# Performance work log

Hardware: AMD Instinct MI355X
Metric: run time of the kernel (lower is better)

## Reference

```python
import jax, jax.numpy as jnp
import numpy as np

ETA = 0.01   # nudging rate from __init__ default
EPS = 1e-8   # cosine-similarity epsilon


def setup_inputs() -> dict:
    key = jax.random.key(0)
    ks = jax.random.split(key, 6)
    B, F, S, E, D = 64, 512, 8192, 500000, 1024
    return {
        "heatmap_features_batch": jax.random.normal(ks[0], (B, F), dtype=jnp.float32),
        "grad_output_batch": jax.random.normal(ks[1], (B, F), dtype=jnp.float32),
        "sign_features": jax.random.normal(ks[2], (S, F), dtype=jnp.float32),
        "edge_weight": jax.random.uniform(ks[3], (E,), dtype=jnp.float32),
        "edge_disease": jax.random.randint(ks[4], (E,), 0, D, dtype=jnp.int32),
        "edge_sign": jax.random.randint(ks[5], (E,), 0, S, dtype=jnp.int32),
        "num_diseases": D,
    }


def reference(heatmap_features_batch, grad_output_batch, sign_features,
              edge_weight, edge_disease, edge_sign, num_diseases):
    # Cosine similarity between every sample's heatmap feature vector and every
    # sign node's stored feature vector, rescaled to [0, 1].
    Hn = heatmap_features_batch / (
        jnp.linalg.norm(heatmap_features_batch, axis=1, keepdims=True) + EPS)
    Sn = sign_features / (
        jnp.linalg.norm(sign_features, axis=1, keepdims=True) + EPS)
    sim = (jnp.einsum('bf,sf->bs', Hn, Sn) + 1.0) * 0.5          # [B, S]

    # Per-edge weighted similarity, gathered at each edge's sign node.
    contrib = sim[:, edge_sign] * edge_weight[None, :]           # [B, E]

    # Scatter-add edge contributions into the disease (source) index.
    agg = jax.ops.segment_sum(contrib.T, edge_disease,
                              num_segments=num_diseases)         # [D, B]

    # Per-sample gradient norm factor g^(i) = ||grad_i||_2.
    gnorm = jnp.linalg.norm(grad_output_batch, axis=1)           # [B]

    return ETA * gnorm[:, None] * agg.T                          # [B, D]
```

## Files before the change

kernel.cpp:

```cpp
#include <hip/hip_runtime.h>
#include <math.h>

#define EPS 1e-8f
#define SCB 256
#define NG1 128
#define CAP 768

typedef __attribute__((ext_vector_type(8))) __bf16 bf16x8;
typedef __attribute__((ext_vector_type(4))) float f32x4;

__device__ __forceinline__ unsigned short f2bf(float x) {
    unsigned int u = __float_as_uint(x);
    u += 0x7FFFu + ((u >> 16) & 1u);
    return (unsigned short)(u >> 16);
}
__device__ __forceinline__ unsigned int pack2(float lo, float hi) {
    return (unsigned int)f2bf(lo) | ((unsigned int)f2bf(hi) << 16);
}

__global__ __launch_bounds__(256) void k_norms(
        const float* __restrict__ Sg, const float* __restrict__ Hg,
        const float* __restrict__ Gg, unsigned short* __restrict__ Sgb,
        unsigned short* __restrict__ Hsb, float* __restrict__ gscale,
        int* __restrict__ cursor, int Srows, int Fdim, int Bdim, int Dd) {
    __shared__ float redA[4][17];
    __shared__ float redB[4][17];
    int bid = blockIdx.x;
    int tid = threadIdx.x;
    int lane = tid & 63, wv = tid >> 6;
    int r = tid & 15, cg = tid >> 4;
    int nsT = Srows >> 4;

    if (bid < nsT + (Bdim >> 4)) {
        bool isH = bid >= nsT;
        int t = isH ? bid - nsT : bid;
        const float* basep = isH ? Hg : Sg;
        const float4* src = (const float4*)(basep + ((size_t)t * 16 + r) * Fdim);

        float4 v[8];
        float ss = 0.f, sgq = 0.f;
        #pragma unroll
        for (int g = 0; g < 4; g++) {
            int c = cg + g * 16;
            float4 x = src[c * 2], y = src[c * 2 + 1];
            v[2 * g] = x; v[2 * g + 1] = y;
            ss += x.x * x.x + x.y * x.y + x.z * x.z + x.w * x.w
                + y.x * y.x + y.y * y.y + y.z * y.z + y.w * y.w;
        }
        if (isH) {
            const float4* srcg = (const float4*)(Gg + ((size_t)t * 16 + r) * Fdim);
            #pragma unroll
            for (int g = 0; g < 4; g++) {
                int c = cg + g * 16;
                float4 x = srcg[c * 2], y = srcg[c * 2 + 1];
                sgq += x.x * x.x + x.y * x.y + x.z * x.z + x.w * x.w
                     + y.x * y.x + y.y * y.y + y.z * y.z + y.w * y.w;
            }
        }
        ss  += __shfl_xor(ss, 16, 64);  ss  += __shfl_xor(ss, 32, 64);
        sgq += __shfl_xor(sgq, 16, 64); sgq += __shfl_xor(sgq, 32, 64);
        if (lane < 16) { redA[wv][lane] = ss; redB[wv][lane] = sgq; }
        __syncthreads();
        float tot = redA[0][r] + redA[1][r] + redA[2][r] + redA[3][r];
        float rv = 1.0f / (sqrtf(tot) + EPS);
        if (isH && tid < 16) {
            float tg = redB[0][tid] + redB[1][tid] + redB[2][tid] + redB[3][tid];
            gscale[t * 16 + tid] = 0.005f * sqrtf(tg);
        }
        uint4* dp = (uint4*)(isH ? Hsb : Sgb);
        #pragma unroll
        for (int g = 0; g < 4; g++) {
            int c = cg + g * 16;
            uint4 o;
            o.x = pack2(v[2 * g].x * rv,     v[2 * g].y * rv);
            o.y = pack2(v[2 * g].z * rv,     v[2 * g].w * rv);
            o.z = pack2(v[2 * g + 1].x * rv, v[2 * g + 1].y * rv);
            o.w = pack2(v[2 * g + 1].z * rv, v[2 * g + 1].w * rv);
            dp[(size_t)t * 1024 + (size_t)c * 16 + r] = o;
        }
    } else {
        for (int i = tid; i < Dd; i += 256) cursor[i] = 0;
    }
}

__global__ __launch_bounds__(256) void k_g1scat(
        const unsigned short* __restrict__ Sgb,
        const unsigned short* __restrict__ Hsb, float* __restrict__ Pt,
        const int* __restrict__ ed, const int* __restrict__ es,
        const float* __restrict__ ew, int* __restrict__ cursor,
        int2* __restrict__ sorted, int Srows, int Fdim, int E, int Dd) {
    __shared__ int cnt[1024];
    int id = blockIdx.x;
    int tid = threadIdx.x;

    if (id < NG1) {
        int lane = tid & 63, w = tid >> 6;
        int wt = id * 4 + w;
        const bf16x8* A  = (const bf16x8*)Sgb + (size_t)wt * 1024 + lane;
        const bf16x8* Bp = (const bf16x8*)Hsb + lane;

        f32x4 acc0 = {0.f, 0.f, 0.f, 0.f};
        f32x4 acc1 = {0.f, 0.f, 0.f, 0.f};
        f32x4 acc2 = {0.f, 0.f, 0.f, 0.f};
        f32x4 acc3 = {0.f, 0.f, 0.f, 0.f};

        #define G1_CHUNK(kc)                                                     \
        {                                                                        \
            bf16x8 a0 = A[(kc) +   0], a1 = A[(kc) +  64];                       \
            bf16x8 a2 = A[(kc) + 128], a3 = A[(kc) + 192];                       \
            bf16x8 b00 = Bp[(kc) +   0], b01 = Bp[(kc) +   0 + 1024];            \
            bf16x8 b02 = Bp[(kc) +   0 + 2048], b03 = Bp[(kc) +   0 + 3072];     \
            bf16x8 b10 = Bp[(kc) +  64], b11 = Bp[(kc) +  64 + 1024];            \
            bf16x8 b12 = Bp[(kc) +  64 + 2048], b13 = Bp[(kc) +  64 + 3072];     \
            bf16x8 b20 = Bp[(kc) + 128], b21 = Bp[(kc) + 128 + 1024];            \
            bf16x8 b22 = Bp[(kc) + 128 + 2048], b23 = Bp[(kc) + 128 + 3072];     \
            bf16x8 b30 = Bp[(kc) + 192], b31 = Bp[(kc) + 192 + 1024];            \
            bf16x8 b32 = Bp[(kc) + 192 + 2048], b33 = Bp[(kc) + 192 + 3072];     \
            acc0 = __builtin_amdgcn_mfma_f32_16x16x32_bf16(a0, b00, acc0, 0, 0, 0); \
            acc1 = __builtin_amdgcn_mfma_f32_16x16x32_bf16(a0, b01, acc1, 0, 0, 0); \
            acc2 = __builtin_amdgcn_mfma_f32_16x16x32_bf16(a0, b02, acc2, 0, 0, 0); \
            acc3 = __builtin_amdgcn_mfma_f32_16x16x32_bf16(a0, b03, acc3, 0, 0, 0); \
            acc0 = __builtin_amdgcn_mfma_f32_16x16x32_bf16(a1, b10, acc0, 0, 0, 0); \
            acc1 = __builtin_amdgcn_mfma_f32_16x16x32_bf16(a1, b11, acc1, 0, 0, 0); \
            acc2 = __builtin_amdgcn_mfma_f32_16x16x32_bf16(a1, b12, acc2, 0, 0, 0); \
            acc3 = __builtin_amdgcn_mfma_f32_16x16x32_bf16(a1, b13, acc3, 0, 0, 0); \
            acc0 = __builtin_amdgcn_mfma_f32_16x16x32_bf16(a2, b20, acc0, 0, 0, 0); \
            acc1 = __builtin_amdgcn_mfma_f32_16x16x32_bf16(a2, b21, acc1, 0, 0, 0); \
            acc2 = __builtin_amdgcn_mfma_f32_16x16x32_bf16(a2, b22, acc2, 0, 0, 0); \
            acc3 = __builtin_amdgcn_mfma_f32_16x16x32_bf16(a2, b23, acc3, 0, 0, 0); \
            acc0 = __builtin_amdgcn_mfma_f32_16x16x32_bf16(a3, b30, acc0, 0, 0, 0); \
            acc1 = __builtin_amdgcn_mfma_f32_16x16x32_bf16(a3, b31, acc1, 0, 0, 0); \
            acc2 = __builtin_amdgcn_mfma_f32_16x16x32_bf16(a3, b32, acc2, 0, 0, 0); \
            acc3 = __builtin_amdgcn_mfma_f32_16x16x32_bf16(a3, b33, acc3, 0, 0, 0); \
        }
        G1_CHUNK(0)
        G1_CHUNK(256)
        G1_CHUNK(512)
        G1_CHUNK(768)
        #undef G1_CHUNK

        int r16 = lane & 15, q = lane >> 4;
        int s0 = wt * 16;
        #pragma unroll
        for (int rr = 0; rr < 4; rr++) {
            int s = s0 + q * 4 + rr;
            float* row = Pt + (size_t)s * 64 + r16;
            row[0]  = acc0[rr];
            row[16] = acc1[rr];
            row[32] = acc2[rr];
            row[48] = acc3[rr];
        }
    } else {
        int h = id - NG1;
        for (int i = tid; i < Dd; i += 256) cnt[i] = 0;
        __syncthreads();
        int chunk = (E + SCB - 1) / SCB;
        int e0 = h * chunk;
        int e1 = min(E, e0 + chunk);
        int myd[8], mys[8], myr[8];
        float myw[8];
        #pragma unroll
        for (int i = 0; i < 8; i++) {
            int e = e0 + tid + i * 256;
            myd[i] = -1;
            if (e < e1) {
                myd[i] = ed[e]; mys[i] = es[e]; myw[i] = ew[e];
                myr[i] = atomicAdd(&cnt[myd[i]], 1);
            }
        }
        __syncthreads();
        for (int d = tid; d < Dd; d += 256) {
            int c = cnt[d];
            if (c) cnt[d] = atomicAdd(&cursor[d], c);
        }
        __syncthreads();
        #pragma unroll
        for (int i = 0; i < 8; i++) {
            if (myd[i] >= 0) {
                int pos = cnt[myd[i]] + myr[i];
                sorted[(size_t)myd[i] * CAP + pos] =
                    make_int2(mys[i], __float_as_int(myw[i]));
            }
        }
    }
}

__global__ __launch_bounds__(512) void k_gather(
        const int2* __restrict__ sorted, const float* __restrict__ Pt,
        const int* __restrict__ cursor, const float* __restrict__ gscale,
        float* __restrict__ out, int Dd) {
    __shared__ float sacc[8][64];
    __shared__ float scs[8];
    int d = blockIdx.x;
    int tid = threadIdx.x;
    int lane = tid & 63, w = tid >> 6;
    int cnt = cursor[d];
    const int2* sp = sorted + (size_t)d * CAP;
    float acc = 0.f, cs = 0.f;
    #pragma unroll 4
    for (int i = w; i < cnt; i += 8) {
        int2 p = sp[i];
        float wt = __int_as_float(p.y);
        acc += wt * Pt[(size_t)p.x * 64 + lane];
        cs += wt;
    }
    sacc[w][lane] = acc;
    if (lane == 0) scs[w] = cs;
    __syncthreads();
    if (tid < 64) {
        float a = sacc[0][tid] + sacc[1][tid] + sacc[2][tid] + sacc[3][tid]
                + sacc[4][tid] + sacc[5][tid] + sacc[6][tid] + sacc[7][tid]
                + scs[0] + scs[1] + scs[2] + scs[3]
                + scs[4] + scs[5] + scs[6] + scs[7];
        out[(size_t)tid * Dd + d] = gscale[tid] * a;
    }
}

extern "C" void kernel_launch(void* const* d_in, const int* in_sizes, int n_in,
                              void* d_out, int out_size, void* d_ws, size_t ws_size,
                              hipStream_t stream) {
    const float* H  = (const float*)d_in[0];
    const float* G  = (const float*)d_in[1];
    const float* Sg = (const float*)d_in[2];
    const float* ew = (const float*)d_in[3];
    const int*   ed = (const int*)d_in[4];
    const int*   es = (const int*)d_in[5];

    const int B = 64;
    const int F = in_sizes[0] / B;
    const int S = in_sizes[2] / F;
    const int E = in_sizes[3];
    const int D = out_size / B;
    float* out = (float*)d_out;

    float* ws = (float*)d_ws;
    size_t off = 0;
    unsigned short* Sgb = (unsigned short*)(ws + off); off += (size_t)S * F / 2;
    unsigned short* Hsb = (unsigned short*)(ws + off); off += (size_t)B * F / 2;
    float* gscale = ws + off; off += 256;
    float* Pt     = ws + off; off += (size_t)S * B;
    int*   cursor = (int*)(ws + off); off += (size_t)D;
    int2*  sorted = (int2*)(ws + off); off += 2 * (size_t)D * CAP;

    k_norms<<<S / 16 + B / 16 + 1, 256, 0, stream>>>(Sg, H, G, Sgb, Hsb, gscale,
                                                     cursor, S, F, B, D);
    k_g1scat<<<NG1 + SCB, 256, 0, stream>>>(Sgb, Hsb, Pt, ed, es, ew,
                                            cursor, sorted, S, F, E, D);
    k_gather<<<D, 512, 0, stream>>>(sorted, Pt, cursor, gscale, out, D);
}
```

Before: 119.1 us.

## Co-schedule edge scatter with normalization kernel, split GEMM into own launch

Moves the edge counting-sort scatter blocks out of the GEMM kernel and into the normalization kernel, so the scatter runs alongside the row-normalization and bf16 conversion instead of alongside the GEMM. The GEMM becomes its own small launch, and cursor zeroing moves to a separate one-block kernel. The aim is to overlap the scatter with the bandwidth-heavy normalization pass and rebalance the pipeline. The cost is one extra kernel launch in total, and the shared-memory reduction buffers are now aliased onto the scatter's shared array.

Result: slower. 123.8 us (+4.0%).

```diff
diff --git a/kernel.cpp b/kernel.cpp
--- a/kernel.cpp
+++ b/kernel.cpp
@@ -18,140 +18,24 @@
     return (unsigned int)f2bf(lo) | ((unsigned int)f2bf(hi) << 16);
 }
 
-__global__ __launch_bounds__(256) void k_norms(
+__global__ __launch_bounds__(256) void k_zero(int* __restrict__ cursor, int Dd) {
+    for (int i = threadIdx.x; i < Dd; i += 256) cursor[i] = 0;
+}
+
+__global__ __launch_bounds__(256) void k0_fused(
         const float* __restrict__ Sg, const float* __restrict__ Hg,
-        const float* __restrict__ Gg, unsigned short* __restrict__ Sgb,
-        unsigned short* __restrict__ Hsb, float* __restrict__ gscale,
-        int* __restrict__ cursor, int Srows, int Fdim, int Bdim, int Dd) {
-    __shared__ float redA[4][17];
-    __shared__ float redB[4][17];
+        const float* __restrict__ Gg, const int* __restrict__ ed,
+        const int* __restrict__ es, const float* __restrict__ ew,
+        unsigned short* __restrict__ Sgb, unsigned short* __restrict__ Hsb,
+        float* __restrict__ gscale, int* __restrict__ cursor,
+        int2* __restrict__ sorted, int Srows, int Fdim, int Bdim, int Dd, int E) {
+    __shared__ int smem[1024];
     int bid = blockIdx.x;
     int tid = threadIdx.x;
-    int lane = tid & 63, wv = tid >> 6;
-    int r = tid & 15, cg = tid >> 4;
-    int nsT = Srows >> 4;
-
-    if (bid < nsT + (Bdim >> 4)) {
-        bool isH = bid >= nsT;
-        int t = isH ? bid - nsT : bid;
-        const float* basep = isH ? Hg : Sg;
-        const float4* src = (const float4*)(basep + ((size_t)t * 16 + r) * Fdim);
-
-        float4 v[8];
-        float ss = 0.f, sgq = 0.f;
-        #pragma unroll
-        for (int g = 0; g < 4; g++) {
-            int c = cg + g * 16;
-            float4 x = src[c * 2], y = src[c * 2 + 1];
-            v[2 * g] = x; v[2 * g + 1] = y;
-            ss += x.x * x.x + x.y * x.y + x.z * x.z + x.w * x.w
-                + y.x * y.x + y.y * y.y + y.z * y.z + y.w * y.w;
-        }
-        if (isH) {
-            const float4* srcg = (const float4*)(Gg + ((size_t)t * 16 + r) * Fdim);
-            #pragma unroll
-            for (int g = 0; g < 4; g++) {
-                int c = cg + g * 16;
-                float4 x = srcg[c * 2], y = srcg[c * 2 + 1];
-                sgq += x.x * x.x + x.y * x.y + x.z * x.z + x.w * x.w
-                     + y.x * y.x + y.y * y.y + y.z * y.z + y.w * y.w;
-            }
-        }
-        ss  += __shfl_xor(ss, 16, 64);  ss  += __shfl_xor(ss, 32, 64);
-        sgq += __shfl_xor(sgq, 16, 64); sgq += __shfl_xor(sgq, 32, 64);
-        if (lane < 16) { redA[wv][lane] = ss; redB[wv][lane] = sgq; }
-        __syncthreads();
-        float tot = redA[0][r] + redA[1][r] + redA[2][r] + redA[3][r];
-        float rv = 1.0f / (sqrtf(tot) + EPS);
-        if (isH && tid < 16) {
-            float tg = redB[0][tid] + redB[1][tid] + redB[2][tid] + redB[3][tid];
-            gscale[t * 16 + tid] = 0.005f * sqrtf(tg);
-        }
-        uint4* dp = (uint4*)(isH ? Hsb : Sgb);
-        #pragma unroll
-        for (int g = 0; g < 4; g++) {
-            int c = cg + g * 16;
-            uint4 o;
-            o.x = pack2(v[2 * g].x * rv,     v[2 * g].y * rv);
-            o.y = pack2(v[2 * g].z * rv,     v[2 * g].w * rv);
-            o.z = pack2(v[2 * g + 1].x * rv, v[2 * g + 1].y * rv);
-            o.w = pack2(v[2 * g + 1].z * rv, v[2 * g + 1].w * rv);
-            dp[(size_t)t * 1024 + (size_t)c * 16 + r] = o;
-        }
-    } else {
-        for (int i = tid; i < Dd; i += 256) cursor[i] = 0;
-    }
-}
-
-__global__ __launch_bounds__(256) void k_g1scat(
-        const unsigned short* __restrict__ Sgb,
-        const unsigned short* __restrict__ Hsb, float* __restrict__ Pt,
-        const int* __restrict__ ed, const int* __restrict__ es,
-        const float* __restrict__ ew, int* __restrict__ cursor,
-        int2* __restrict__ sorted, int Srows, int Fdim, int E, int Dd) {
-    __shared__ int cnt[1024];
-    int id = blockIdx.x;
-    int tid = threadIdx.x;
-
-    if (id < NG1) {
-        int lane = tid & 63, w = tid >> 6;
-        int wt = id * 4 + w;
-        const bf16x8* A  = (const bf16x8*)Sgb + (size_t)wt * 1024 + lane;
-        const bf16x8* Bp = (const bf16x8*)Hsb + lane;
-
-        f32x4 acc0 = {0.f, 0.f, 0.f, 0.f};
-        f32x4 acc1 = {0.f, 0.f, 0.f, 0.f};
-        f32x4 acc2 = {0.f, 0.f, 0.f, 0.f};
-        f32x4 acc3 = {0.f, 0.f, 0.f, 0.f};
-
-        #define G1_CHUNK(kc)                                                     \
-        {                                                                        \
-            bf16x8 a0 = A[(kc) +   0], a1 = A[(kc) +  64];                       \
-            bf16x8 a2 = A[(kc) + 128], a3 = A[(kc) + 192];                       \
-            bf16x8 b00 = Bp[(kc) +   0], b01 = Bp[(kc) +   0 + 1024];            \
-            bf16x8 b02 = Bp[(kc) +   0 + 2048], b03 = Bp[(kc) +   0 + 3072];     \
-            bf16x8 b10 = Bp[(kc) +  64], b11 = Bp[(kc) +  64 + 1024];            \
-            bf16x8 b12 = Bp[(kc) +  64 + 2048], b13 = Bp[(kc) +  64 + 3072];     \
-            bf16x8 b20 = Bp[(kc) + 128], b21 = Bp[(kc) + 128 + 1024];            \
-            bf16x8 b22 = Bp[(kc) + 128 + 2048], b23 = Bp[(kc) + 128 + 3072];     \
-            bf16x8 b30 = Bp[(kc) + 192], b31 = Bp[(kc) + 192 + 1024];            \
-            bf16x8 b32 = Bp[(kc) + 192 + 2048], b33 = Bp[(kc) + 192 + 3072];     \
-            acc0 = __builtin_amdgcn_mfma_f32_16x16x32_bf16(a0, b00, acc0, 0, 0, 0); \
-            acc1 = __builtin_amdgcn_mfma_f32_16x16x32_bf16(a0, b01, acc1, 0, 0, 0); \
-            acc2 = __builtin_amdgcn_mfma_f32_16x16x32_bf16(a0, b02, acc2, 0, 0, 0); \
-            acc3 = __builtin_amdgcn_mfma_f32_16x16x32_bf16(a0, b03, acc3, 0, 0, 0); \
-            acc0 = __builtin_amdgcn_mfma_f32_16x16x32_bf16(a1, b10, acc0, 0, 0, 0); \
-            acc1 = __builtin_amdgcn_mfma_f32_16x16x32_bf16(a1, b11, acc1, 0, 0, 0); \
-            acc2 = __builtin_amdgcn_mfma_f32_16x16x32_bf16(a1, b12, acc2, 0, 0, 0); \
-            acc3 = __builtin_amdgcn_mfma_f32_16x16x32_bf16(a1, b13, acc3, 0, 0, 0); \
-            acc0 = __builtin_amdgcn_mfma_f32_16x16x32_bf16(a2, b20, acc0, 0, 0, 0); \
-            acc1 = __builtin_amdgcn_mfma_f32_16x16x32_bf16(a2, b21, acc1, 0, 0, 0); \
-            acc2 = __builtin_amdgcn_mfma_f32_16x16x32_bf16(a2, b22, acc2, 0, 0, 0); \
-            acc3 = __builtin_amdgcn_mfma_f32_16x16x32_bf16(a2, b23, acc3, 0, 0, 0); \
-            acc0 = __builtin_amdgcn_mfma_f32_16x16x32_bf16(a3, b30, acc0, 0, 0, 0); \
-            acc1 = __builtin_amdgcn_mfma_f32_16x16x32_bf16(a3, b31, acc1, 0, 0, 0); \
-            acc2 = __builtin_amdgcn_mfma_f32_16x16x32_bf16(a3, b32, acc2, 0, 0, 0); \
-            acc3 = __builtin_amdgcn_mfma_f32_16x16x32_bf16(a3, b33, acc3, 0, 0, 0); \
-        }
-        G1_CHUNK(0)
-        G1_CHUNK(256)
-        G1_CHUNK(512)
-        G1_CHUNK(768)
-        #undef G1_CHUNK
-
-        int r16 = lane & 15, q = lane >> 4;
-        int s0 = wt * 16;
-        #pragma unroll
-        for (int rr = 0; rr < 4; rr++) {
-            int s = s0 + q * 4 + rr;
-            float* row = Pt + (size_t)s * 64 + r16;
-            row[0]  = acc0[rr];
-            row[16] = acc1[rr];
-            row[32] = acc2[rr];
-            row[48] = acc3[rr];
-        }
-    } else {
-        int h = id - NG1;
+
+    if (bid < SCB) {
+        int* cnt = smem;
+        int h = bid;
         for (int i = tid; i < Dd; i += 256) cnt[i] = 0;
         __syncthreads();
         int chunk = (E + SCB - 1) / SCB;
@@ -182,6 +66,125 @@
                     make_int2(mys[i], __float_as_int(myw[i]));
             }
         }
+        return;
+    }
+
+    float (*redA)[17] = (float (*)[17])smem;
+    float (*redB)[17] = (float (*)[17])(smem + 68);
+    int lane = tid & 63, wv = tid >> 6;
+    int r = tid & 15, cg = tid >> 4;
+    int nsT = Srows >> 4;
+    int nb = bid - SCB;
+    if (nb >= nsT + (Bdim >> 4)) return;
+
+    bool isH = nb >= nsT;
+    int t = isH ? nb - nsT : nb;
+    const float* basep = isH ? Hg : Sg;
+    const float4* src = (const float4*)(basep + ((size_t)t * 16 + r) * Fdim);
+
+    float4 v[8];
+    float ss = 0.f, sgq = 0.f;
+    #pragma unroll
+    for (int g = 0; g < 4; g++) {
+        int c = cg + g * 16;
+        float4 x = src[c * 2], y = src[c * 2 + 1];
+        v[2 * g] = x; v[2 * g + 1] = y;
+        ss += x.x * x.x + x.y * x.y + x.z * x.z + x.w * x.w
+            + y.x * y.x + y.y * y.y + y.z * y.z + y.w * y.w;
+    }
+    if (isH) {
+        const float4* srcg = (const float4*)(Gg + ((size_t)t * 16 + r) * Fdim);
+        #pragma unroll
+        for (int g = 0; g < 4; g++) {
+            int c = cg + g * 16;
+            float4 x = srcg[c * 2], y = srcg[c * 2 + 1];
+            sgq += x.x * x.x + x.y * x.y + x.z * x.z + x.w * x.w
+                 + y.x * y.x + y.y * y.y + y.z * y.z + y.w * y.w;
+        }
+    }
+    ss  += __shfl_xor(ss, 16, 64);  ss  += __shfl_xor(ss, 32, 64);
+    sgq += __shfl_xor(sgq, 16, 64); sgq += __shfl_xor(sgq, 32, 64);
+    if (lane < 16) { redA[wv][lane] = ss; redB[wv][lane] = sgq; }
+    __syncthreads();
+    float tot = redA[0][r] + redA[1][r] + redA[2][r] + redA[3][r];
+    float rv = 1.0f / (sqrtf(tot) + EPS);
+    if (isH && tid < 16) {
+        float tg = redB[0][tid] + redB[1][tid] + redB[2][tid] + redB[3][tid];
+        gscale[t * 16 + tid] = 0.005f * sqrtf(tg);
+    }
+    uint4* dp = (uint4*)(isH ? Hsb : Sgb);
+    #pragma unroll
+    for (int g = 0; g < 4; g++) {
+        int c = cg + g * 16;
+        uint4 o;
+        o.x = pack2(v[2 * g].x * rv,     v[2 * g].y * rv);
+        o.y = pack2(v[2 * g].z * rv,     v[2 * g].w * rv);
+        o.z = pack2(v[2 * g + 1].x * rv, v[2 * g + 1].y * rv);
+        o.w = pack2(v[2 * g + 1].z * rv, v[2 * g + 1].w * rv);
+        dp[(size_t)t * 1024 + (size_t)c * 16 + r] = o;
+    }
+}
+
+__global__ __launch_bounds__(256) void k_gemm(
+        const unsigned short* __restrict__ Sgb,
+        const unsigned short* __restrict__ Hsb, float* __restrict__ Pt,
+        int Srows, int Fdim) {
+    int tid = threadIdx.x;
+    int lane = tid & 63, w = tid >> 6;
+    int wt = blockIdx.x * 4 + w;
+    const bf16x8* A  = (const bf16x8*)Sgb + (size_t)wt * 1024 + lane;
+    const bf16x8* Bp = (const bf16x8*)Hsb + lane;
+
+    f32x4 acc0 = {0.f, 0.f, 0.f, 0.f};
+    f32x4 acc1 = {0.f, 0.f, 0.f, 0.f};
+    f32x4 acc2 = {0.f, 0.f, 0.f, 0.f};
+    f32x4 acc3 = {0.f, 0.f, 0.f, 0.f};
+
+    #define G1_CHUNK(kc)                                                     \
+    {                                                                        \
+        bf16x8 a0 = A[(kc) +   0], a1 = A[(kc) +  64];                       \
+        bf16x8 a2 = A[(kc) + 128], a3 = A[(kc) + 192];                       \
+        bf16x8 b00 = Bp[(kc) +   0], b01 = Bp[(kc) +   0 + 1024];            \
+        bf16x8 b02 = Bp[(kc) +   0 + 2048], b03 = Bp[(kc) +   0 + 3072];     \
+        bf16x8 b10 = Bp[(kc) +  64], b11 = Bp[(kc) +  64 + 1024];            \
+        bf16x8 b12 = Bp[(kc) +  64 + 2048], b13 = Bp[(kc) +  64 + 3072];     \
+        bf16x8 b20 = Bp[(kc) + 128], b21 = Bp[(kc) + 128 + 1024];            \
+        bf16x8 b22 = Bp[(kc) + 128 + 2048], b23 = Bp[(kc) + 128 + 3072];     \
+        bf16x8 b30 = Bp[(kc) + 192], b31 = Bp[(kc) + 192 + 1024];            \
+        bf16x8 b32 = Bp[(kc) + 192 + 2048], b33 = Bp[(kc) + 192 + 3072];     \
+        acc0 = __builtin_amdgcn_mfma_f32_16x16x32_bf16(a0, b00, acc0, 0, 0, 0); \
+        acc1 = __builtin_amdgcn_mfma_f32_16x16x32_bf16(a0, b01, acc1, 0, 0, 0); \
+        acc2 = __builtin_amdgcn_mfma_f32_16x16x32_bf16(a0, b02, acc2, 0, 0, 0); \
+        acc3 = __builtin_amdgcn_mfma_f32_16x16x32_bf16(a0, b03, acc3, 0, 0, 0); \
+        acc0 = __builtin_amdgcn_mfma_f32_16x16x32_bf16(a1, b10, acc0, 0, 0, 0); \
+        acc1 = __builtin_amdgcn_mfma_f32_16x16x32_bf16(a1, b11, acc1, 0, 0, 0); \
+        acc2 = __builtin_amdgcn_mfma_f32_16x16x32_bf16(a1, b12, acc2, 0, 0, 0); \
+        acc3 = __builtin_amdgcn_mfma_f32_16x16x32_bf16(a1, b13, acc3, 0, 0, 0); \
+        acc0 = __builtin_amdgcn_mfma_f32_16x16x32_bf16(a2, b20, acc0, 0, 0, 0); \
+        acc1 = __builtin_amdgcn_mfma_f32_16x16x32_bf16(a2, b21, acc1, 0, 0, 0); \
+        acc2 = __builtin_amdgcn_mfma_f32_16x16x32_bf16(a2, b22, acc2, 0, 0, 0); \
+        acc3 = __builtin_amdgcn_mfma_f32_16x16x32_bf16(a2, b23, acc3, 0, 0, 0); \
+        acc0 = __builtin_amdgcn_mfma_f32_16x16x32_bf16(a3, b30, acc0, 0, 0, 0); \
+        acc1 = __builtin_amdgcn_mfma_f32_16x16x32_bf16(a3, b31, acc1, 0, 0, 0); \
+        acc2 = __builtin_amdgcn_mfma_f32_16x16x32_bf16(a3, b32, acc2, 0, 0, 0); \
+        acc3 = __builtin_amdgcn_mfma_f32_16x16x32_bf16(a3, b33, acc3, 0, 0, 0); \
+    }
+    G1_CHUNK(0)
+    G1_CHUNK(256)
+    G1_CHUNK(512)
+    G1_CHUNK(768)
+    #undef G1_CHUNK
+
+    int r16 = lane & 15, q = lane >> 4;
+    int s0 = wt * 16;
+    #pragma unroll
+    for (int rr = 0; rr < 4; rr++) {
+        int s = s0 + q * 4 + rr;
+        float* row = Pt + (size_t)s * 64 + r16;
+        row[0]  = acc0[rr];
+        row[16] = acc1[rr];
+        row[32] = acc2[rr];
+        row[48] = acc3[rr];
     }
 }
 
@@ -242,9 +245,9 @@
     int*   cursor = (int*)(ws + off); off += (size_t)D;
     int2*  sorted = (int2*)(ws + off); off += 2 * (size_t)D * CAP;
 
-    k_norms<<<S / 16 + B / 16 + 1, 256, 0, stream>>>(Sg, H, G, Sgb, Hsb, gscale,
-                                                     cursor, S, F, B, D);
-    k_g1scat<<<NG1 + SCB, 256, 0, stream>>>(Sgb, Hsb, Pt, ed, es, ew,
-                                            cursor, sorted, S, F, E, D);
+    k_zero<<<1, 256, 0, stream>>>(cursor, D);
+    k0_fused<<<SCB + S / 16 + B / 16, 256, 0, stream>>>(
+        Sg, H, G, ed, es, ew, Sgb, Hsb, gscale, cursor, sorted, S, F, B, D, E);
+    k_gemm<<<NG1, 256, 0, stream>>>(Sgb, Hsb, Pt, S, F);
     k_gather<<<D, 512, 0, stream>>>(sorted, Pt, cursor, gscale, out, D);
 }
```
